# Performance work log

Measured on AMD Instinct MI355X. Metric: run time of the kernel, lower is better.

Reference implementation:

```python
import jax, jax.numpy as jnp
import numpy as np

B, T, D, V, MEM = 2, 512, 512, 256, 256


def _gru(x, h0, wih, whh, bih, bhh):
    # x: [B,T,D], h0: [B,D]; torch GRU gate order: r, z, n
    def step(h, xt):
        gi = xt @ wih.T + bih            # [B,3D]
        gh = h @ whh.T + bhh             # [B,3D]
        i_r, i_z, i_n = jnp.split(gi, 3, axis=-1)
        h_r, h_z, h_n = jnp.split(gh, 3, axis=-1)
        r = jax.nn.sigmoid(i_r + h_r)
        z = jax.nn.sigmoid(i_z + h_z)
        n = jnp.tanh(i_n + r * h_n)
        h_new = (1.0 - z) * n + z * h
        return h_new, h_new
    hT, ys = jax.lax.scan(step, h0, jnp.swapaxes(x, 0, 1))
    return jnp.swapaxes(ys, 0, 1), hT


def _layernorm(x, g, b, eps=1e-5):
    m = jnp.mean(x, axis=-1, keepdims=True)
    v = jnp.mean((x - m) ** 2, axis=-1, keepdims=True)
    return (x - m) / jnp.sqrt(v + eps) * g + b


def setup_inputs() -> dict:
    key = jax.random.key(0)
    ks = jax.random.split(key, 24)
    s = 1.0 / np.sqrt(D)
    inp = {
        'x': jax.random.randint(ks[0], (B, T), 0, V, dtype=jnp.int32),
        'h_f': jnp.zeros((1, B, D), jnp.float32),
        'h_s': jnp.zeros((1, B, D), jnp.float32),
        'soma_w': jax.random.normal(ks[1], (V, D), jnp.float32),
        'fast_wih': jax.random.normal(ks[2], (3 * D, D)) * s,
        'fast_whh': jax.random.normal(ks[3], (3 * D, D)) * s,
        'fast_bih': jax.random.normal(ks[4], (3 * D,)) * s,
        'fast_bhh': jax.random.normal(ks[5], (3 * D,)) * s,
        'slow_wih': jax.random.normal(ks[6], (3 * D, D)) * s,
        'slow_whh': jax.random.normal(ks[7], (3 * D, D)) * s,
        'slow_bih': jax.random.normal(ks[8], (3 * D,)) * s,
        'slow_bhh': jax.random.normal(ks[9], (3 * D,)) * s,
        'qkv_w': jax.random.normal(ks[10], (3 * D, D)) * s,
        'qkv_b': jax.random.normal(ks[11], (3 * D,)) * s,
        'gate_w': jax.random.normal(ks[12], (D, D)) * s,
        'gate_b': jax.random.normal(ks[13], (D,)) * s,
        'gate_g': jnp.ones((D,), jnp.float32),
        'gate_bb': jnp.zeros((D,), jnp.float32),
        'mem_bank': jax.random.normal(ks[14], (MEM, D)) * 0.1,
        'hip_qw': jax.random.normal(ks[15], (D, D)) * s,
        'hip_qb': jax.random.normal(ks[16], (D,)) * s,
        'axon_w': jax.random.normal(ks[17], (D, 4 * D)) * (0.5 * s),
        'axon_b': jax.random.normal(ks[18], (D,)) * s,
        'norm_g': jnp.ones((D,), jnp.float32),
        'norm_b': jnp.zeros((D,), jnp.float32),
    }
    return inp


def reference(x, h_f, h_s, soma_w, fast_wih, fast_whh, fast_bih, fast_bhh,
              slow_wih, slow_whh, slow_bih, slow_bhh, qkv_w, qkv_b,
              gate_w, gate_b, gate_g, gate_bb, mem_bank, hip_qw, hip_qb,
              axon_w, axon_b, norm_g, norm_b):
    d = soma_w.shape[1]
    s_in = soma_w[x]  # mod[0] == 1.0
    p_f, hf1 = _gru(s_in, h_f[0], fast_wih, fast_whh, fast_bih, fast_bhh)
    p_s, hs1 = _gru(p_f, h_s[0], slow_wih, slow_whh, slow_bih, slow_bhh)
    # LinearIntentMemory: naive cumulative outer-product linear attention
    qkv = p_s @ qkv_w.T + qkv_b
    q, k, v = jnp.split(qkv, 3, axis=-1)
    q = jax.nn.elu(q) + 1.0
    k = jax.nn.elu(k) + 1.0
    kv_cum = jnp.cumsum(jnp.einsum('bti,btj->btij', k, v), axis=1)  # [B,T,D,D]
    num = jnp.einsum('bti,btij->btj', q, kv_cum)
    den = jnp.einsum('bti,bti->bt', q, jnp.cumsum(k, axis=1))[..., None] + 1e-6
    l_mem = num / den
    # intent gate: Linear -> LayerNorm -> Tanh
    intent = jnp.tanh(_layernorm(p_s @ gate_w.T + gate_b, gate_g, gate_bb))
    # hippocampus: softmax attention over memory bank
    qh = p_s @ hip_qw.T + hip_qb
    attn = qh @ mem_bank.T / jnp.sqrt(jnp.float32(d))
    episodes = jax.nn.softmax(attn, axis=-1) @ mem_bank
    combined = jnp.concatenate([p_f, intent, l_mem, episodes], axis=-1)
    thought = _layernorm(jnp.tanh(combined @ axon_w.T + axon_b), norm_g, norm_b)
    sw = soma_w / jnp.maximum(jnp.linalg.norm(soma_w, axis=-1, keepdims=True), 1e-12)
    logits = (thought @ sw.T) * 16.0
    return (logits, thought, hf1[None], hs1[None])
```

## Files before the change

### kernel.cpp

```cpp
#include <hip/hip_runtime.h>
#include <cstddef>

#define F_ELUQK 1
#define F_CAUSAL 2
#define F_DIV 4
#define F_NN 8
#define F_SCALE 16
#define F_ROWSUM 32
#define FLAG_STRIDE 32
#define L_WGS 64
#define UNITS 8

enum : int {
  OFF_QH = 0,
  OFF_GI = 524288,
  OFF_COMB = OFF_GI + 1572864,
  OFF_PS = OFF_COMB + 2097152,
  OFF_QKV = OFF_PS + 524288,
  OFF_SCORES = OFF_QKV + 1572864,
  OFF_DEN = OFF_SCORES + 524288,
  OFF_TMP = OFF_DEN + 1024,
  OFF_ATTN = OFF_TMP + 524288,
  OFF_SWN = OFF_ATTN + 262144,
  OFF_RING = OFF_SWN + 256,
  OFF_HSB = OFF_RING + 4096,
  OFF_FLAGS = OFF_HSB + 2048
};

__global__ __launch_bounds__(256) void gemm(
    const float* __restrict__ A, int lda, const float* __restrict__ B, int ldb,
    float* __restrict__ C, int ldc, int coff, int K,
    const float* __restrict__ bias, const float* __restrict__ den,
    const float* __restrict__ cscale, float* __restrict__ rsum,
    float scale, int flags, int bBatch, const int* __restrict__ xidx,
    float* __restrict__ Cz, int kzoff) {
  __shared__ float As[16 * 65];
  __shared__ float Bs[16 * 65];
  int tid = threadIdx.x;
  int n0 = blockIdx.x * 64, m0 = blockIdx.y * 64;
  if (blockIdx.z) { A += kzoff; B += kzoff; C = Cz; bias = nullptr; }
  int rowoff = (m0 >> 9) * bBatch;
  int tx = tid & 15, ty = tid >> 4;

  if ((flags & F_CAUSAL) && n0 > ((m0 & 511) + 63)) {
    #pragma unroll
    for (int i = 0; i < 4; ++i)
      #pragma unroll
      for (int j = 0; j < 4; ++j)
        C[(size_t)(m0 + ty * 4 + i) * ldc + coff + n0 + tx * 4 + j] = 0.f;
    return;
  }

  float acc[4][4] = {};
  for (int k0 = 0; k0 < K; k0 += 16) {
    {
      int rr = tid >> 2, c4 = (tid & 3) << 2;
      int arow = m0 + rr;
      const float* ap = xidx ? (A + (size_t)xidx[arow] * 512 + (k0 + c4))
                             : (A + (size_t)arow * lda + (k0 + c4));
      float4 av = *(const float4*)ap;
      As[(c4 + 0) * 65 + rr] = av.x;
      As[(c4 + 1) * 65 + rr] = av.y;
      As[(c4 + 2) * 65 + rr] = av.z;
      As[(c4 + 3) * 65 + rr] = av.w;
    }
    if (!(flags & F_NN)) {
      int rr = tid >> 2, c4 = (tid & 3) << 2;
      const float* bp = B + (size_t)(n0 + rr + rowoff) * ldb + (k0 + c4);
      float4 bv = *(const float4*)bp;
      Bs[(c4 + 0) * 65 + rr] = bv.x; Bs[(c4 + 1) * 65 + rr] = bv.y;
      Bs[(c4 + 2) * 65 + rr] = bv.z; Bs[(c4 + 3) * 65 + rr] = bv.w;
    } else {
      int kk = tid >> 4, n4 = (tid & 15) << 2;
      const float* bp = B + (size_t)(k0 + kk + rowoff) * ldb + (n0 + n4);
      float4 bv = *(const float4*)bp;
      Bs[kk * 65 + n4 + 0] = bv.x; Bs[kk * 65 + n4 + 1] = bv.y;
      Bs[kk * 65 + n4 + 2] = bv.z; Bs[kk * 65 + n4 + 3] = bv.w;
    }
    __syncthreads();
    #pragma unroll
    for (int k = 0; k < 16; ++k) {
      float av[4], bv[4];
      #pragma unroll
      for (int i = 0; i < 4; ++i) av[i] = As[k * 65 + ty * 4 + i];
      #pragma unroll
      for (int j = 0; j < 4; ++j) bv[j] = Bs[k * 65 + tx * 4 + j];
      #pragma unroll
      for (int i = 0; i < 4; ++i)
        #pragma unroll
        for (int j = 0; j < 4; ++j)
          acc[i][j] = fmaf(av[i], bv[j], acc[i][j]);
    }
    __syncthreads();
  }
  float rs[4] = {0.f, 0.f, 0.f, 0.f};
  #pragma unroll
  for (int i = 0; i < 4; ++i) {
    int m = m0 + ty * 4 + i;
    float dv = (flags & F_DIV) ? (1.0f / (den[m] + 1e-6f)) : 1.0f;
    #pragma unroll
    for (int j = 0; j < 4; ++j) {
      int n = n0 + tx * 4 + j;
      float v = acc[i][j];
      if (bias) v += bias[n];
      if (flags & F_ELUQK) { if (n < 1024) v = (v > 0.f) ? (v + 1.f) : __expf(v); }
      if (flags & F_CAUSAL) { if (n > (m & 511)) v = 0.f; }
      if (flags & F_SCALE) v *= scale;
      if (cscale) v *= cscale[coff + n];
      if (flags & F_DIV) v *= dv;
      C[(size_t)m * ldc + coff + n] = v;
      if (flags & F_ROWSUM) rs[i] += v;
    }
  }
  if (flags & F_ROWSUM) {
    #pragma unroll
    for (int i = 0; i < 4; ++i) {
      float s = rs[i];
      s += __shfl_xor(s, 1); s += __shfl_xor(s, 2);
      s += __shfl_xor(s, 4); s += __shfl_xor(s, 8);
      if (tx == 0) atomicAdd(rsum + (m0 + ty * 4 + i), s);
    }
  }
}

__global__ __launch_bounds__(256) void gemm3(
    const float* __restrict__ A,
    const float* __restrict__ qkvw, const float* __restrict__ qkvb,
    const float* __restrict__ gatew, const float* __restrict__ gateb,
    const float* __restrict__ hipw, const float* __restrict__ hipb,
    float* __restrict__ QKV, float* __restrict__ TMP, float* __restrict__ QH) {
  __shared__ float As[16 * 65];
  __shared__ float Bs[16 * 65];
  int tid = threadIdx.x;
  int n0 = blockIdx.x * 64, m0 = blockIdx.y * 64;
  const float* B; const float* bias; float* C; int ldc, base;
  if (n0 < 1536) { B = qkvw; bias = qkvb; C = QKV; ldc = 1536; base = 0; }
  else if (n0 < 2048) { B = gatew; bias = gateb; C = TMP; ldc = 512; base = 1536; }
  else { B = hipw; bias = hipb; C = QH; ldc = 512; base = 2048; }
  int tx = tid & 15, ty = tid >> 4;
  float acc[4][4] = {};
  for (int k0 = 0; k0 < 512; k0 += 16) {
    {
      int rr = tid >> 2, c4 = (tid & 3) << 2;
      const float* ap = A + (size_t)(m0 + rr) * 512 + (k0 + c4);
      float4 av = *(const float4*)ap;
      As[(c4 + 0) * 65 + rr] = av.x; As[(c4 + 1) * 65 + rr] = av.y;
      As[(c4 + 2) * 65 + rr] = av.z; As[(c4 + 3) * 65 + rr] = av.w;
    }
    {
      int rr = tid >> 2, c4 = (tid & 3) << 2;
      const float* bp = B + (size_t)(n0 - base + rr) * 512 + (k0 + c4);
      float4 bv = *(const float4*)bp;
      Bs[(c4 + 0) * 65 + rr] = bv.x; Bs[(c4 + 1) * 65 + rr] = bv.y;
      Bs[(c4 + 2) * 65 + rr] = bv.z; Bs[(c4 + 3) * 65 + rr] = bv.w;
    }
    __syncthreads();
    #pragma unroll
    for (int k = 0; k < 16; ++k) {
      float av[4], bv[4];
      #pragma unroll
      for (int i = 0; i < 4; ++i) av[i] = As[k * 65 + ty * 4 + i];
      #pragma unroll
      for (int j = 0; j < 4; ++j) bv[j] = Bs[k * 65 + tx * 4 + j];
      #pragma unroll
      for (int i = 0; i < 4; ++i)
        #pragma unroll
        for (int j = 0; j < 4; ++j)
          acc[i][j] = fmaf(av[i], bv[j], acc[i][j]);
    }
    __syncthreads();
  }
  #pragma unroll
  for (int i = 0; i < 4; ++i) {
    int m = m0 + ty * 4 + i;
    #pragma unroll
    for (int j = 0; j < 4; ++j) {
      int n = n0 + tx * 4 + j;
      float v = acc[i][j] + bias[n - base];
      if (n < 1024) v = (v > 0.f) ? (v + 1.f) : __expf(v);
      C[(size_t)m * ldc + (n - base)] = v;
    }
  }
}

__device__ __forceinline__ void post_flag(unsigned* flags, int w, unsigned v) {
  __hip_atomic_store(flags + (size_t)w * FLAG_STRIDE, v, __ATOMIC_RELAXED,
                     __HIP_MEMORY_SCOPE_AGENT);
}
__device__ __forceinline__ void poll64(const unsigned* flags, unsigned tgt, int lane) {
  const unsigned* p = flags + (size_t)lane * FLAG_STRIDE;
  while (__hip_atomic_load(p, __ATOMIC_RELAXED, __HIP_MEMORY_SCOPE_AGENT) < tgt)
    __builtin_amdgcn_s_sleep(1);
}

__global__ __launch_bounds__(256, 1) void gru2_kernel(
    const float* __restrict__ gi,
    const float* __restrict__ fwhh, const float* __restrict__ fbhh,
    const float* __restrict__ h0f,
    const float* __restrict__ swih, const float* __restrict__ sbih,
    const float* __restrict__ swhh, const float* __restrict__ sbhh,
    const float* __restrict__ h0s,
    float* __restrict__ pf_out,
    float* __restrict__ ps_out,
    float* __restrict__ hfT, float* __restrict__ hsT,
    float* __restrict__ ring,
    float* __restrict__ hsbuf,
    unsigned* __restrict__ flagsA, unsigned* __restrict__ flagsB) {
  __shared__ __attribute__((aligned(16))) float hl[1024];
  __shared__ __attribute__((aligned(16))) float hfs[1024];
  __shared__ float P[48];
  __shared__ float Q[48];
  __shared__ float bl[24];
  __shared__ float bi[24];
  int tid = threadIdx.x, wg = blockIdx.x;
  bool L1 = wg < L_WGS;
  int j0 = (wg & (L_WGS - 1)) * UNITS;
  int part = tid & 7, r = tid >> 3;
  int g = r >> 3, u = r & 7;
  int wave = tid >> 6, lane = tid & 63;
  const float* whh = L1 ? fwhh : swhh;
  const float* bhh = L1 ? fbhh : sbhh;

  float4 wh[16], wi[16];
  if (r < 24) {
    const float* wp = whh + (size_t)(g * 512 + j0 + u) * 512 + part * 4;
    #pragma unroll
    for (int i = 0; i < 16; ++i) wh[i] = *(const float4*)(wp + i * 32);
    if (!L1) {
      const float* wp2 = swih + (size_t)(g * 512 + j0 + u) * 512 + part * 4;
      #pragma unroll
      for (int i = 0; i < 16; ++i) wi[i] = *(const float4*)(wp2 + i * 32);
    }
  }
  if (tid < 24) {
    bl[tid] = bhh[(tid >> 3) * 512 + j0 + (tid & 7)];
    if (!L1) bi[tid] = sbih[(tid >> 3) * 512 + j0 + (tid & 7)];
  }

  unsigned long long* hlq = (unsigned long long*)hl;
  unsigned long long* hfq = (unsigned long long*)hfs;
  const float4* h4 = (const float4*)hl;
  const float4* f4v = (const float4*)hfs;

  if (L1) {
    for (int t = 0; t < 512; ++t) {
      float i_r = 0.f, i_z = 0.f, i_n = 0.f;
      if (tid < 16) {
        int b = tid >> 3, jl = tid & 7;
        const float* girow = gi + (size_t)(b * 512 + t) * 1536 + j0 + jl;
        i_r = girow[0]; i_z = girow[512]; i_n = girow[1024];
      }
      if (wave == 0) {
        if (t > 0) poll64(flagsA, (unsigned)t, lane);
        unsigned long long v[8];
        if (t == 0) {
          const unsigned long long* s8 = (const unsigned long long*)h0f;
          #pragma unroll
          for (int k = 0; k < 8; ++k) v[k] = s8[k * 64 + lane];
        } else {
          const unsigned long long* s8 =
              (const unsigned long long*)(ring + ((t - 1) & 3) * 1024);
          #pragma unroll
          for (int k = 0; k < 8; ++k)
            v[k] = __hip_atomic_load(s8 + k * 64 + lane, __ATOMIC_RELAXED,
                                     __HIP_MEMORY_SCOPE_AGENT);
        }
        #pragma unroll
        for (int k = 0; k < 8; ++k) hlq[k * 64 + lane] = v[k];
      } else if (wave == 1) {
        if (t >= 4) poll64(flagsB, (unsigned)(t - 3), lane);
      }
      __syncthreads();
      if (r < 24) {
        float a0 = 0.f, a1 = 0.f;
        #pragma unroll
        for (int i = 0; i < 16; ++i) {
          float4 w = wh[i];
          float4 x0 = h4[i * 8 + part];
          float4 x1 = h4[128 + i * 8 + part];
          a0 += w.x * x0.x + w.y * x0.y + w.z * x0.z + w.w * x0.w;
          a1 += w.x * x1.x + w.y * x1.y + w.z * x1.z + w.w * x1.w;
        }
        a0 += __shfl_xor(a0, 1); a0 += __shfl_xor(a0, 2); a0 += __shfl_xor(a0, 4);
        a1 += __shfl_xor(a1, 1); a1 += __shfl_xor(a1, 2); a1 += __shfl_xor(a1, 4);
        if (part == 0) { P[r] = a0; P[24 + r] = a1; }
      }
      __syncthreads();
      if (tid < 16) {
        int b = tid >> 3, u2 = tid & 7, j = j0 + u2;
        float gh_r = P[b * 24 + u2] + bl[u2];
        float gh_z = P[b * 24 + 8 + u2] + bl[8 + u2];
        float gh_n = P[b * 24 + 16 + u2] + bl[16 + u2];
        float hold = hl[b * 512 + j];
        float rg = 1.0f / (1.0f + __expf(-(i_r + gh_r)));
        float zg = 1.0f / (1.0f + __expf(-(i_z + gh_z)));
        float ng = tanhf(i_n + rg * gh_n);
        float hnew = (1.0f - zg) * ng + zg * hold;
        __hip_atomic_store(ring + (size_t)(t & 3) * 1024 + b * 512 + j, hnew,
                           __ATOMIC_RELAXED, __HIP_MEMORY_SCOPE_AGENT);
        pf_out[(size_t)(b * 512 + t) * 2048 + j] = hnew;
        if (t == 511) hfT[b * 512 + j] = hnew;
      }
      __syncthreads();
      if (tid == 0) post_flag(flagsA, wg, (unsigned)(t + 1));
    }
  } else {
    for (int t2 = 0; t2 < 512; ++t2) {
      if (wave == 0) {
        poll64(flagsA, (unsigned)(t2 + 1), lane);
        const unsigned long long* f8 =
            (const unsigned long long*)(ring + (t2 & 3) * 1024);
        unsigned long long v[8];
        #pragma unroll
        for (int k = 0; k < 8; ++k)
          v[k] = __hip_atomic_load(f8 + k * 64 + lane, __ATOMIC_RELAXED,
                                   __HIP_MEMORY_SCOPE_AGENT);
        #pragma unroll
        for (int k = 0; k < 8; ++k) hfq[k * 64 + lane] = v[k];
      } else if (wave == 1) {
        unsigned long long v[8];
        if (t2 == 0) {
          const unsigned long long* s8 = (const unsigned long long*)h0s;
          #pragma unroll
          for (int k = 0; k < 8; ++k) v[k] = s8[k * 64 + lane];
        } else {
          poll64(flagsB, (unsigned)t2, lane);
          const unsigned long long* s8 =
              (const unsigned long long*)(hsbuf + ((t2 - 1) & 1) * 1024);
          #pragma unroll
          for (int k = 0; k < 8; ++k)
            v[k] = __hip_atomic_load(s8 + k * 64 + lane, __ATOMIC_RELAXED,
                                     __HIP_MEMORY_SCOPE_AGENT);
        }
        #pragma unroll
        for (int k = 0; k < 8; ++k) hlq[k * 64 + lane] = v[k];
      }
      __syncthreads();
      if (r < 24) {
        float a0 = 0.f, a1 = 0.f, c0 = 0.f, c1 = 0.f;
        #pragma unroll
        for (int i = 0; i < 16; ++i) {
          float4 w = wh[i];
          float4 x0 = h4[i * 8 + part];
          float4 x1 = h4[128 + i * 8 + part];
          a0 += w.x * x0.x + w.y * x0.y + w.z * x0.z + w.w * x0.w;
          a1 += w.x * x1.x + w.y * x1.y + w.z * x1.z + w.w * x1.w;
          float4 v = wi[i];
          float4 y0 = f4v[i * 8 + part];
          float4 y1 = f4v[128 + i * 8 + part];
          c0 += v.x * y0.x + v.y * y0.y + v.z * y0.z + v.w * y0.w;
          c1 += v.x * y1.x + v.y * y1.y + v.z * y1.z + v.w * y1.w;
        }
        a0 += __shfl_xor(a0, 1); a0 += __shfl_xor(a0, 2); a0 += __shfl_xor(a0, 4);
        a1 += __shfl_xor(a1, 1); a1 += __shfl_xor(a1, 2); a1 += __shfl_xor(a1, 4);
        c0 += __shfl_xor(c0, 1); c0 += __shfl_xor(c0, 2); c0 += __shfl_xor(c0, 4);
        c1 += __shfl_xor(c1, 1); c1 += __shfl_xor(c1, 2); c1 += __shfl_xor(c1, 4);
        if (part == 0) { P[r] = a0; P[24 + r] = a1; Q[r] = c0; Q[24 + r] = c1; }
      }
      __syncthreads();
      if (tid < 16) {
        int b = tid >> 3, u2 = tid & 7, j = j0 + u2;
        float i_r = Q[b * 24 + u2] + bi[u2];
        float i_z = Q[b * 24 + 8 + u2] + bi[8 + u2];
        float i_n = Q[b * 24 + 16 + u2] + bi[16 + u2];
        float gh_r = P[b * 24 + u2] + bl[u2];
        float gh_z = P[b * 24 + 8 + u2] + bl[8 + u2];
        float gh_n = P[b * 24 + 16 + u2] + bl[16 + u2];
        float hold = hl[b * 512 + j];
        float rg = 1.0f / (1.0f + __expf(-(i_r + gh_r)));
        float zg = 1.0f / (1.0f + __expf(-(i_z + gh_z)));
        float ng = tanhf(i_n + rg * gh_n);
        float hnew = (1.0f - zg) * ng + zg * hold;
        __hip_atomic_store(hsbuf + (size_t)(t2 & 1) * 1024 + b * 512 + j, hnew,
                           __ATOMIC_RELAXED, __HIP_MEMORY_SCOPE_AGENT);
        ps_out[(size_t)(b * 512 + t2) * 512 + j] = hnew;
        if (t2 == 511) hsT[b * 512 + j] = hnew;
      }
      __syncthreads();
      if (tid == 0) post_flag(flagsB, wg - L_WGS, (unsigned)(t2 + 1));
    }
  }
}

__global__ __launch_bounds__(256) void softmax_kernel(float* __restrict__ a) {
  int m = blockIdx.x, tid = threadIdx.x;
  float v = a[(size_t)m * 256 + tid];
  float mx = v;
  #pragma unroll
  for (int off = 32; off > 0; off >>= 1) mx = fmaxf(mx, __shfl_down(mx, off));
  __shared__ float r4[4];
  __shared__ float s4[4];
  if ((tid & 63) == 0) r4[tid >> 6] = mx;
  __syncthreads();
  mx = fmaxf(fmaxf(r4[0], r4[1]), fmaxf(r4[2], r4[3]));
  float e = __expf(v - mx);
  float s = e;
  #pragma unroll
  for (int off = 32; off > 0; off >>= 1) s += __shfl_down(s, off);
  if ((tid & 63) == 0) s4[tid >> 6] = s;
  __syncthreads();
  s = s4[0] + s4[1] + s4[2] + s4[3];
  a[(size_t)m * 256 + tid] = e / s;
}

__global__ __launch_bounds__(256) void ln_kernel(
    const float* __restrict__ src, const float* __restrict__ src2,
    float* __restrict__ dst, int ldd, int dcoff,
    const float* __restrict__ gv, const float* __restrict__ bv, int tanhFirst) {
  int m = blockIdx.x, tid = threadIdx.x;
  float x0 = src[(size_t)m * 512 + tid];
  float x1 = src[(size_t)m * 512 + 256 + tid];
  if (src2) { x0 += src2[(size_t)m * 512 + tid]; x1 += src2[(size_t)m * 512 + 256 + tid]; }
  if (tanhFirst) { x0 = tanhf(x0); x1 = tanhf(x1); }
  float s = x0 + x1, ss = x0 * x0 + x1 * x1;
  #pragma unroll
  for (int off = 32; off > 0; off >>= 1) { s += __shfl_down(s, off); ss += __shfl_down(ss, off); }
  __shared__ float rs[4], rss[4];
  if ((tid & 63) == 0) { rs[tid >> 6] = s; rss[tid >> 6] = ss; }
  __syncthreads();
  float st = rs[0] + rs[1] + rs[2] + rs[3];
  float sst = rss[0] + rss[1] + rss[2] + rss[3];
  float mean = st * (1.0f / 512.0f);
  float var = sst * (1.0f / 512.0f) - mean * mean;
  float inv = rsqrtf(var + 1e-5f);
  float y0 = (x0 - mean) * inv * gv[tid] + bv[tid];
  float y1 = (x1 - mean) * inv * gv[256 + tid] + bv[256 + tid];
  if (!tanhFirst) { y0 = tanhf(y0); y1 = tanhf(y1); }
  dst[(size_t)m * ldd + dcoff + tid] = y0;
  dst[(size_t)m * ldd + dcoff + 256 + tid] = y1;
}

__global__ __launch_bounds__(256) void swinv_kernel(const float* __restrict__ soma,
                                                    float* __restrict__ swn) {
  int r = blockIdx.x, tid = threadIdx.x;
  float x0 = soma[(size_t)r * 512 + tid];
  float x1 = soma[(size_t)r * 512 + 256 + tid];
  float ss = x0 * x0 + x1 * x1;
  #pragma unroll
  for (int off = 32; off > 0; off >>= 1) ss += __shfl_down(ss, off);
  __shared__ float r4[4];
  if ((tid & 63) == 0) r4[tid >> 6] = ss;
  __syncthreads();
  if (tid == 0) {
    float norm = fmaxf(sqrtf(r4[0] + r4[1] + r4[2] + r4[3]), 1e-12f);
    swn[r] = 16.0f / norm;
  }
}

extern "C" void kernel_launch(void* const* d_in, const int* in_sizes, int n_in,
                              void* d_out, int out_size, void* d_ws, size_t ws_size,
                              hipStream_t stream) {
  (void)in_sizes; (void)n_in; (void)out_size; (void)ws_size;
  float* W = (float*)d_ws;
  float* outf = (float*)d_out;
  const int* x = (const int*)d_in[0];
  const float* soma = (const float*)d_in[3];

  hipMemsetAsync((char*)d_ws + (size_t)OFF_FLAGS * 4, 0, 16384, stream);
  hipMemsetAsync((char*)d_ws + (size_t)OFF_DEN * 4, 0, 4096, stream);

  gemm<<<dim3(24, 16), 256, 0, stream>>>(soma, 512, (const float*)d_in[4], 512,
      W + OFF_GI, 1536, 0, 512, (const float*)d_in[6], nullptr, nullptr, nullptr,
      1.f, 0, 0, x, nullptr, 0);

  gru2_kernel<<<2 * L_WGS, 256, 0, stream>>>(W + OFF_GI,
      (const float*)d_in[5], (const float*)d_in[7], (const float*)d_in[1],
      (const float*)d_in[8], (const float*)d_in[10],
      (const float*)d_in[9], (const float*)d_in[11], (const float*)d_in[2],
      W + OFF_COMB, W + OFF_PS, outf + 786432, outf + 787456,
      W + OFF_RING, W + OFF_HSB,
      (unsigned*)(W + OFF_FLAGS), (unsigned*)(W + OFF_FLAGS) + L_WGS * FLAG_STRIDE);

  gemm3<<<dim3(40, 16), 256, 0, stream>>>(W + OFF_PS,
      (const float*)d_in[12], (const float*)d_in[13],
      (const float*)d_in[14], (const float*)d_in[15],
      (const float*)d_in[19], (const float*)d_in[20],
      W + OFF_QKV, W + OFF_TMP, W + OFF_QH);

  gemm<<<dim3(8, 16), 256, 0, stream>>>(W + OFF_QKV, 1536, W + OFF_QKV + 512, 1536,
      W + OFF_SCORES, 512, 0, 512, nullptr, nullptr, nullptr, W + OFF_DEN,
      1.f, F_CAUSAL | F_ROWSUM, 512, nullptr, nullptr, 0);

  gemm<<<dim3(8, 16), 256, 0, stream>>>(W + OFF_SCORES, 512, W + OFF_QKV + 1024, 1536,
      W + OFF_COMB, 2048, 1024, 512, nullptr, W + OFF_DEN, nullptr, nullptr,
      1.f, F_NN | F_DIV, 512, nullptr, nullptr, 0);

  ln_kernel<<<1024, 256, 0, stream>>>(W + OFF_TMP, nullptr, W + OFF_COMB, 2048, 512,
      (const float*)d_in[16], (const float*)d_in[17], 0);

  gemm<<<dim3(4, 16), 256, 0, stream>>>(W + OFF_QH, 512, (const float*)d_in[18], 512,
      W + OFF_ATTN, 256, 0, 512, nullptr, nullptr, nullptr, nullptr,
      0.04419417382415922f, F_SCALE, 0, nullptr, nullptr, 0);
  softmax_kernel<<<1024, 256, 0, stream>>>(W + OFF_ATTN);
  gemm<<<dim3(8, 16), 256, 0, stream>>>(W + OFF_ATTN, 256, (const float*)d_in[18], 512,
      W + OFF_COMB, 2048, 1536, 256, nullptr, nullptr, nullptr, nullptr,
      1.f, F_NN, 0, nullptr, nullptr, 0);

  gemm<<<dim3(8, 16, 2), 256, 0, stream>>>(W + OFF_COMB, 2048, (const float*)d_in[21], 2048,
      W + OFF_TMP, 512, 0, 1024, (const float*)d_in[22], nullptr, nullptr, nullptr,
      1.f, 0, 0, nullptr, W + OFF_QH, 1024);

  ln_kernel<<<1024, 256, 0, stream>>>(W + OFF_TMP, W + OFF_QH, outf + 262144, 512, 0,
      (const float*)d_in[23], (const float*)d_in[24], 1);

  swinv_kernel<<<256, 256, 0, stream>>>(soma, W + OFF_SWN);
  gemm<<<dim3(4, 16), 256, 0, stream>>>(outf + 262144, 512, soma, 512,
      outf, 256, 0, 512, nullptr, nullptr, W + OFF_SWN, nullptr,
      1.f, 0, 0, nullptr, nullptr, 0);
}
```

Before: 2.028 ms.

## Fuse fast-GRU input projection into recurrent kernel with register-resident weights

Removes the separate gather+GEMM that precomputed the fast GRU's input gates, and instead has each layer-1 workgroup hold its slice of W_ih in registers and compute x_t·W_ih per step. Two spare waves prefetch the next timestep's embedding row into a double-buffered shared array, hiding the gather behind the recurrence. This drops one kernel launch and the GI workspace round-trip, at the cost of extra per-step FMA work and register pressure on the latency-critical serial loop.

```diff
diff --git a/kernel.cpp b/kernel.cpp
--- a/kernel.cpp
+++ b/kernel.cpp
@@ -13,8 +13,7 @@
 
 enum : int {
   OFF_QH = 0,
-  OFF_GI = 524288,
-  OFF_COMB = OFF_GI + 1572864,
+  OFF_COMB = 524288,
   OFF_PS = OFF_COMB + 2097152,
   OFF_QKV = OFF_PS + 524288,
   OFF_SCORES = OFF_QKV + 1572864,
@@ -32,7 +31,7 @@
     float* __restrict__ C, int ldc, int coff, int K,
     const float* __restrict__ bias, const float* __restrict__ den,
     const float* __restrict__ cscale, float* __restrict__ rsum,
-    float scale, int flags, int bBatch, const int* __restrict__ xidx,
+    float scale, int flags, int bBatch,
     float* __restrict__ Cz, int kzoff) {
   __shared__ float As[16 * 65];
   __shared__ float Bs[16 * 65];
@@ -55,9 +54,7 @@
   for (int k0 = 0; k0 < K; k0 += 16) {
     {
       int rr = tid >> 2, c4 = (tid & 3) << 2;
-      int arow = m0 + rr;
-      const float* ap = xidx ? (A + (size_t)xidx[arow] * 512 + (k0 + c4))
-                             : (A + (size_t)arow * lda + (k0 + c4));
+      const float* ap = A + (size_t)(m0 + rr) * lda + (k0 + c4);
       float4 av = *(const float4*)ap;
       As[(c4 + 0) * 65 + rr] = av.x;
       As[(c4 + 1) * 65 + rr] = av.y;
@@ -194,7 +191,8 @@
 }
 
 __global__ __launch_bounds__(256, 1) void gru2_kernel(
-    const float* __restrict__ gi,
+    const float* __restrict__ soma, const int* __restrict__ x,
+    const float* __restrict__ fwih, const float* __restrict__ fbih,
     const float* __restrict__ fwhh, const float* __restrict__ fbhh,
     const float* __restrict__ h0f,
     const float* __restrict__ swih, const float* __restrict__ sbih,
@@ -207,11 +205,12 @@
     float* __restrict__ hsbuf,
     unsigned* __restrict__ flagsA, unsigned* __restrict__ flagsB) {
   __shared__ __attribute__((aligned(16))) float hl[1024];
-  __shared__ __attribute__((aligned(16))) float hfs[1024];
+  __shared__ __attribute__((aligned(16))) float inb[2048];
   __shared__ float P[48];
   __shared__ float Q[48];
   __shared__ float bl[24];
   __shared__ float bi[24];
+  __shared__ int xl[1024];
   int tid = threadIdx.x, wg = blockIdx.x;
   bool L1 = wg < L_WGS;
   int j0 = (wg & (L_WGS - 1)) * UNITS;
@@ -220,36 +219,33 @@
   int wave = tid >> 6, lane = tid & 63;
   const float* whh = L1 ? fwhh : swhh;
   const float* bhh = L1 ? fbhh : sbhh;
+  const float* wih = L1 ? fwih : swih;
+  const float* bih = L1 ? fbih : sbih;
 
   float4 wh[16], wi[16];
   if (r < 24) {
     const float* wp = whh + (size_t)(g * 512 + j0 + u) * 512 + part * 4;
     #pragma unroll
     for (int i = 0; i < 16; ++i) wh[i] = *(const float4*)(wp + i * 32);
-    if (!L1) {
-      const float* wp2 = swih + (size_t)(g * 512 + j0 + u) * 512 + part * 4;
-      #pragma unroll
-      for (int i = 0; i < 16; ++i) wi[i] = *(const float4*)(wp2 + i * 32);
-    }
+    const float* wp2 = wih + (size_t)(g * 512 + j0 + u) * 512 + part * 4;
+    #pragma unroll
+    for (int i = 0; i < 16; ++i) wi[i] = *(const float4*)(wp2 + i * 32);
   }
   if (tid < 24) {
     bl[tid] = bhh[(tid >> 3) * 512 + j0 + (tid & 7)];
-    if (!L1) bi[tid] = sbih[(tid >> 3) * 512 + j0 + (tid & 7)];
-  }
+    bi[tid] = bih[(tid >> 3) * 512 + j0 + (tid & 7)];
+  }
+  if (L1) {
+    for (int q = tid; q < 1024; q += 256) xl[q] = x[q];
+  }
+  __syncthreads();
 
   unsigned long long* hlq = (unsigned long long*)hl;
-  unsigned long long* hfq = (unsigned long long*)hfs;
+  unsigned long long* inq = (unsigned long long*)inb;
   const float4* h4 = (const float4*)hl;
-  const float4* f4v = (const float4*)hfs;
 
   if (L1) {
     for (int t = 0; t < 512; ++t) {
-      float i_r = 0.f, i_z = 0.f, i_n = 0.f;
-      if (tid < 16) {
-        int b = tid >> 3, jl = tid & 7;
-        const float* girow = gi + (size_t)(b * 512 + t) * 1536 + j0 + jl;
-        i_r = girow[0]; i_z = girow[512]; i_n = girow[1024];
-      }
       if (wave == 0) {
         if (t > 0) poll64(flagsA, (unsigned)t, lane);
         unsigned long long v[8];
@@ -269,10 +265,25 @@
         for (int k = 0; k < 8; ++k) hlq[k * 64 + lane] = v[k];
       } else if (wave == 1) {
         if (t >= 4) poll64(flagsB, (unsigned)(t - 3), lane);
+      } else {
+        int b = wave - 2;
+        if (t == 0) {
+          int row0 = xl[b * 512];
+          const float4* sp = (const float4*)(soma + (size_t)row0 * 512);
+          float4* dst = (float4*)(inb + b * 512);
+          dst[lane * 2] = sp[lane * 2]; dst[lane * 2 + 1] = sp[lane * 2 + 1];
+        }
+        if (t + 1 < 512) {
+          int row = xl[b * 512 + t + 1];
+          const float4* sp = (const float4*)(soma + (size_t)row * 512);
+          float4* dst = (float4*)(inb + ((t + 1) & 1) * 1024 + b * 512);
+          dst[lane * 2] = sp[lane * 2]; dst[lane * 2 + 1] = sp[lane * 2 + 1];
+        }
       }
       __syncthreads();
       if (r < 24) {
-        float a0 = 0.f, a1 = 0.f;
+        const float4* f4v = (const float4*)(inb + (t & 1) * 1024);
+        float a0 = 0.f, a1 = 0.f, c0 = 0.f, c1 = 0.f;
         #pragma unroll
         for (int i = 0; i < 16; ++i) {
           float4 w = wh[i];
@@ -280,14 +291,24 @@
           float4 x1 = h4[128 + i * 8 + part];
           a0 += w.x * x0.x + w.y * x0.y + w.z * x0.z + w.w * x0.w;
           a1 += w.x * x1.x + w.y * x1.y + w.z * x1.z + w.w * x1.w;
+          float4 v = wi[i];
+          float4 y0 = f4v[i * 8 + part];
+          float4 y1 = f4v[128 + i * 8 + part];
+          c0 += v.x * y0.x + v.y * y0.y + v.z * y0.z + v.w * y0.w;
+          c1 += v.x * y1.x + v.y * y1.y + v.z * y1.z + v.w * y1.w;
         }
         a0 += __shfl_xor(a0, 1); a0 += __shfl_xor(a0, 2); a0 += __shfl_xor(a0, 4);
         a1 += __shfl_xor(a1, 1); a1 += __shfl_xor(a1, 2); a1 += __shfl_xor(a1, 4);
-        if (part == 0) { P[r] = a0; P[24 + r] = a1; }
+        c0 += __shfl_xor(c0, 1); c0 += __shfl_xor(c0, 2); c0 += __shfl_xor(c0, 4);
+        c1 += __shfl_xor(c1, 1); c1 += __shfl_xor(c1, 2); c1 += __shfl_xor(c1, 4);
+        if (part == 0) { P[r] = a0; P[24 + r] = a1; Q[r] = c0; Q[24 + r] = c1; }
       }
       __syncthreads();
       if (tid < 16) {
         int b = tid >> 3, u2 = tid & 7, j = j0 + u2;
+        float i_r = Q[b * 24 + u2] + bi[u2];
+        float i_z = Q[b * 24 + 8 + u2] + bi[8 + u2];
+        float i_n = Q[b * 24 + 16 + u2] + bi[16 + u2];
         float gh_r = P[b * 24 + u2] + bl[u2];
         float gh_z = P[b * 24 + 8 + u2] + bl[8 + u2];
         float gh_n = P[b * 24 + 16 + u2] + bl[16 + u2];
@@ -316,7 +337,7 @@
           v[k] = __hip_atomic_load(f8 + k * 64 + lane, __ATOMIC_RELAXED,
                                    __HIP_MEMORY_SCOPE_AGENT);
         #pragma unroll
-        for (int k = 0; k < 8; ++k) hfq[k * 64 + lane] = v[k];
+        for (int k = 0; k < 8; ++k) inq[(t2 & 1) * 512 + k * 64 + lane] = v[k];
       } else if (wave == 1) {
         unsigned long long v[8];
         if (t2 == 0) {
@@ -337,6 +358,7 @@
       }
       __syncthreads();
       if (r < 24) {
+        const float4* f4v = (const float4*)(inb + (t2 & 1) * 1024);
         float a0 = 0.f, a1 = 0.f, c0 = 0.f, c1 = 0.f;
         #pragma unroll
         for (int i = 0; i < 16; ++i) {
@@ -459,11 +481,8 @@
   hipMemsetAsync((char*)d_ws + (size_t)OFF_FLAGS * 4, 0, 16384, stream);
   hipMemsetAsync((char*)d_ws + (size_t)OFF_DEN * 4, 0, 4096, stream);
 
-  gemm<<<dim3(24, 16), 256, 0, stream>>>(soma, 512, (const float*)d_in[4], 512,
-      W + OFF_GI, 1536, 0, 512, (const float*)d_in[6], nullptr, nullptr, nullptr,
-      1.f, 0, 0, x, nullptr, 0);
-
-  gru2_kernel<<<2 * L_WGS, 256, 0, stream>>>(W + OFF_GI,
+  gru2_kernel<<<2 * L_WGS, 256, 0, stream>>>(soma, x,
+      (const float*)d_in[4], (const float*)d_in[6],
       (const float*)d_in[5], (const float*)d_in[7], (const float*)d_in[1],
       (const float*)d_in[8], (const float*)d_in[10],
       (const float*)d_in[9], (const float*)d_in[11], (const float*)d_in[2],
@@ -479,26 +498,26 @@
 
   gemm<<<dim3(8, 16), 256, 0, stream>>>(W + OFF_QKV, 1536, W + OFF_QKV + 512, 1536,
       W + OFF_SCORES, 512, 0, 512, nullptr, nullptr, nullptr, W + OFF_DEN,
-      1.f, F_CAUSAL | F_ROWSUM, 512, nullptr, nullptr, 0);
+      1.f, F_CAUSAL | F_ROWSUM, 512, nullptr, 0);
 
   gemm<<<dim3(8, 16), 256, 0, stream>>>(W + OFF_SCORES, 512, W + OFF_QKV + 1024, 1536,
       W + OFF_COMB, 2048, 1024, 512, nullptr, W + OFF_DEN, nullptr, nullptr,
-      1.f, F_NN | F_DIV, 512, nullptr, nullptr, 0);
+      1.f, F_NN | F_DIV, 512, nullptr, 0);
 
   ln_kernel<<<1024, 256, 0, stream>>>(W + OFF_TMP, nullptr, W + OFF_COMB, 2048, 512,
       (const float*)d_in[16], (const float*)d_in[17], 0);
 
   gemm<<<dim3(4, 16), 256, 0, stream>>>(W + OFF_QH, 512, (const float*)d_in[18], 512,
       W + OFF_ATTN, 256, 0, 512, nullptr, nullptr, nullptr, nullptr,
-      0.04419417382415922f, F_SCALE, 0, nullptr, nullptr, 0);
+      0.04419417382415922f, F_SCALE, 0, nullptr, 0);
   softmax_kernel<<<1024, 256, 0, stream>>>(W + OFF_ATTN);
   gemm<<<dim3(8, 16), 256, 0, stream>>>(W + OFF_ATTN, 256, (const float*)d_in[18], 512,
       W + OFF_COMB, 2048, 1536, 256, nullptr, nullptr, nullptr, nullptr,
-      1.f, F_NN, 0, nullptr, nullptr, 0);
+      1.f, F_NN, 0, nullptr, 0);
 
   gemm<<<dim3(8, 16, 2), 256, 0, stream>>>(W + OFF_COMB, 2048, (const float*)d_in[21], 2048,
       W + OFF_TMP, 512, 0, 1024, (const float*)d_in[22], nullptr, nullptr, nullptr,
-      1.f, 0, 0, nullptr, W + OFF_QH, 1024);
+      1.f, 0, 0, W + OFF_QH, 1024);
 
   ln_kernel<<<1024, 256, 0, stream>>>(W + OFF_TMP, W + OFF_QH, outf + 262144, 512, 0,
       (const float*)d_in[23], (const float*)d_in[24], 1);
@@ -506,5 +525,5 @@
   swinv_kernel<<<256, 256, 0, stream>>>(soma, W + OFF_SWN);
   gemm<<<dim3(4, 16), 256, 0, stream>>>(outf + 262144, 512, soma, 512,
       outf, 256, 0, 512, nullptr, nullptr, W + OFF_SWN, nullptr,
-      1.f, 0, 0, nullptr, nullptr, 0);
-}
+      1.f, 0, 0, nullptr, 0);
+}
```

Measured after the change: 2.024 ms. No clear change (-0.2%).
